# Kernel tuning notes

Measured on AMD Instinct MI355X. Metric: run time of the kernel, lower is better.

Reference implementation:

```python
import jax, jax.numpy as jnp
import numpy as np

E, K, MULT = 8, 2, 4          # num_experts, top_k, ffn mult
CF = 1.25                     # capacity_factor


def setup_inputs() -> dict:
    key = jax.random.key(0)
    ks = jax.random.split(key, 8)
    B, T, C = 4, 2048, 1024
    H = C * MULT
    s = 0.02
    return {
        "x": jax.random.normal(ks[0], (B, T, C), jnp.float32),
        "rw": jax.random.normal(ks[1], (E, C), jnp.float32) * s,   # router weight [E,C]
        "rb": jnp.zeros((E,), jnp.float32),                        # router bias
        "w1": jax.random.normal(ks[2], (E, C, H), jnp.float32) * s,
        "b1": jnp.zeros((E, H), jnp.float32),
        "w2": jax.random.normal(ks[3], (E, H, C), jnp.float32) * s,
        "b2": jnp.zeros((E, C), jnp.float32),
    }


def reference(x, rw, rb, w1, b1, w2, b2):
    B, T, C = x.shape
    N = B * T
    cap = int(CF * N / E)                      # static capacity per expert
    xf = x.reshape(N, C)
    logits = xf @ rw.T + rb                    # [N,E]
    probs = jax.nn.softmax(logits, axis=-1)
    topk_probs, topk_idx = jax.lax.top_k(probs, K)      # [N,K]
    topk_probs = topk_probs / topk_probs.sum(-1, keepdims=True)

    # Flatten (token, choice) row-major == torch.where(mask) ordering
    flat_idx = topk_idx.reshape(-1)            # [N*K] expert id per slot
    flat_gate = topk_probs.reshape(-1)         # [N*K]
    onehot = jax.nn.one_hot(flat_idx, E, dtype=jnp.int32)          # [N*K,E]
    pos = (jnp.cumsum(onehot, axis=0) - 1)[jnp.arange(N * K), flat_idx]  # rank within expert
    keep = pos < cap                           # first-come-first-served capacity drop
    tok = jnp.arange(N * K) // K               # owning token of each slot

    # Dispatch into [E, cap] buffers; dropped slots go to a dump slot at the end
    buf = jnp.where(keep, flat_idx * cap + pos, E * cap)
    gate_buf = jnp.zeros(E * cap + 1, x.dtype).at[buf].add(flat_gate)[:E * cap]
    tok_buf = jnp.zeros(E * cap + 1, jnp.int32).at[buf].set(tok)[:E * cap]

    inp = xf[tok_buf].reshape(E, cap, C)       # gathered expert inputs
    h = jax.nn.gelu(jnp.einsum('eic,ech->eih', inp, w1) + b1[:, None, :], approximate=False)
    out = jnp.einsum('eih,ehc->eic', h, w2) + b2[:, None, :]
    out = out * gate_buf.reshape(E, cap, 1)    # empty slots have gate 0 -> zero contribution

    y = jnp.zeros((N, C), x.dtype).at[tok_buf].add(out.reshape(E * cap, C))

    # Aux load-balancing loss
    imp = probs.sum(0)
    imp = imp / imp.sum()
    load = jnp.minimum(onehot.sum(0).astype(x.dtype), cap)   # kept token counts
    load = load / load.sum()
    aux_loss = (imp * load).sum() * (E ** 2)
    return y.reshape(B, T, C), aux_loss
```

## Files before the change

### kernel.cpp

```cpp
#include <hip/hip_runtime.h>
#include <hip/hip_bf16.h>
#include <math.h>

#define NE    8
#define KTOP  2
#define CDIM  1024
#define HDIM  4096
#define NTOK  8192
#define CAPE  1280
#define NSLOT (NTOK * KTOP)

typedef __bf16 bf16x8 __attribute__((ext_vector_type(8)));
typedef __bf16 bf16x4 __attribute__((ext_vector_type(4)));
typedef float  f32x4  __attribute__((ext_vector_type(4)));

#define GAS __attribute__((address_space(1)))
#define LAS __attribute__((address_space(3)))

__device__ __forceinline__ void transpose64_body(
    const float* __restrict__ src, __bf16* __restrict__ dst, int R, int Cc,
    int bx, int by, int e, int t, char* sm)
{
    __bf16 (*T)[72] = (__bf16(*)[72])sm;
    const int cb = bx * 64;
    const int rb = by * 64;
    const int px = t & 15, py = t >> 4;

    const float* s = src + (size_t)e * R * Cc
                   + (size_t)(rb + py * 4) * Cc + cb + px * 4;
    float4 m[4];
#pragma unroll
    for (int i = 0; i < 4; ++i)
        m[i] = *(const float4*)(s + (size_t)i * Cc);
#pragma unroll
    for (int j = 0; j < 4; ++j) {
        bf16x4 v;
        v[0] = (__bf16)((&m[0].x)[j]);
        v[1] = (__bf16)((&m[1].x)[j]);
        v[2] = (__bf16)((&m[2].x)[j]);
        v[3] = (__bf16)((&m[3].x)[j]);
        *(bf16x4*)&T[px * 4 + j][py * 4] = v;
    }
    __syncthreads();
    const int oc = t >> 2, rc = (t & 3) * 16;
    __bf16* d = dst + (size_t)e * R * Cc + (size_t)(cb + oc) * R + rb + rc;
    *(bf16x8*)d       = *(const bf16x8*)&T[oc][rc];
    *(bf16x8*)(d + 8) = *(const bf16x8*)&T[oc][rc + 8];
}

__global__ __launch_bounds__(256) void k_prolog(
    const float* __restrict__ w1, const float* __restrict__ w2,
    const float* __restrict__ x, const float* __restrict__ rw,
    const float* __restrict__ rb,
    __bf16* __restrict__ w1t, __bf16* __restrict__ w2t,
    float* __restrict__ probs, float* __restrict__ gates,
    int* __restrict__ tidx)
{
    __shared__ char sm[32768];
    const int bid = blockIdx.x;
    const int t   = threadIdx.x;

    if (bid < 8192) {
        const int bx = bid & 63, by = (bid >> 6) & 15, e = bid >> 10;
        transpose64_body(w1, w1t, CDIM, HDIM, bx, by, e, t, sm);
        return;
    }
    if (bid < 16384) {
        const int b2 = bid - 8192;
        const int bx = b2 & 15, by = (b2 >> 4) & 63, e = b2 >> 10;
        transpose64_body(w2, w2t, HDIM, CDIM, bx, by, e, t, sm);
        return;
    }

    float* rws = (float*)sm;
    for (int i = t; i < NE * CDIM / 4; i += 256)
        ((float4*)rws)[i] = ((const float4*)rw)[i];
    __syncthreads();

    const int wave = t >> 6, lane = t & 63;
    const int n = (bid - 16384) * 4 + wave;
    const float* xr = x + (size_t)n * CDIM;

    float acc[NE];
#pragma unroll
    for (int e = 0; e < NE; ++e) acc[e] = 0.f;
    for (int j = 0; j < CDIM / 64; ++j) {
        const float xv = xr[j * 64 + lane];
#pragma unroll
        for (int e = 0; e < NE; ++e) acc[e] += xv * rws[e * CDIM + j * 64 + lane];
    }
#pragma unroll
    for (int off = 32; off > 0; off >>= 1) {
#pragma unroll
        for (int e = 0; e < NE; ++e) acc[e] += __shfl_down(acc[e], off);
    }
    if (lane == 0) {
        float mx = -1e30f;
#pragma unroll
        for (int e = 0; e < NE; ++e) { acc[e] += rb[e]; mx = fmaxf(mx, acc[e]); }
        float p[NE], s = 0.f;
#pragma unroll
        for (int e = 0; e < NE; ++e) { p[e] = expf(acc[e] - mx); s += p[e]; }
        const float inv = 1.f / s;
#pragma unroll
        for (int e = 0; e < NE; ++e) { p[e] *= inv; probs[(size_t)n * NE + e] = p[e]; }
        int   i1 = 0;  float v1 = p[0];
        int   i2 = -1; float v2 = -1.f;
#pragma unroll
        for (int e = 1; e < NE; ++e) {
            if (p[e] > v1)      { v2 = v1; i2 = i1; v1 = p[e]; i1 = e; }
            else if (p[e] > v2) { v2 = p[e]; i2 = e; }
        }
        const float gs = 1.f / (v1 + v2);
        gates[n * 2 + 0] = v1 * gs;  gates[n * 2 + 1] = v2 * gs;
        tidx[n * 2 + 0]  = i1;       tidx[n * 2 + 1]  = i2;
    }
}

__global__ __launch_bounds__(256) void k_scan(
    const int* __restrict__ tidx, const float* __restrict__ probs,
    int* __restrict__ slot, int* __restrict__ tok, float* __restrict__ d_aux)
{
    __shared__ int   lcnt[256][NE];
    __shared__ float ps[256][NE];
    const int t = threadIdx.x;

    for (int i = t; i < NE * CAPE; i += 256) tok[i] = 0;

    int c8[NE];
#pragma unroll
    for (int e = 0; e < NE; ++e) c8[e] = 0;
    const int per  = NSLOT / 256;
    const int base = t * per;
    for (int s = 0; s < per; ++s) c8[tidx[base + s]]++;
#pragma unroll
    for (int e = 0; e < NE; ++e) lcnt[t][e] = c8[e];

    float f8[NE];
#pragma unroll
    for (int e = 0; e < NE; ++e) f8[e] = 0.f;
    for (int n = t; n < NTOK; n += 256) {
        const float4 a = *(const float4*)(probs + (size_t)n * NE);
        const float4 b = *(const float4*)(probs + (size_t)n * NE + 4);
        f8[0] += a.x; f8[1] += a.y; f8[2] += a.z; f8[3] += a.w;
        f8[4] += b.x; f8[5] += b.y; f8[6] += b.z; f8[7] += b.w;
    }
#pragma unroll
    for (int e = 0; e < NE; ++e) ps[t][e] = f8[e];

    __syncthreads();

    int run[NE];
#pragma unroll
    for (int e = 0; e < NE; ++e) run[e] = c8[e];
    for (int d = 1; d < 256; d <<= 1) {
        int add[NE];
#pragma unroll
        for (int e = 0; e < NE; ++e) add[e] = (t >= d) ? lcnt[t - d][e] : 0;
        __syncthreads();
#pragma unroll
        for (int e = 0; e < NE; ++e) { run[e] += add[e]; lcnt[t][e] = run[e]; }
        __syncthreads();
    }
    int pre[NE], tot[NE];
#pragma unroll
    for (int e = 0; e < NE; ++e) {
        pre[e] = run[e] - c8[e];
        tot[e] = lcnt[255][e];
    }

    for (int d = 128; d >= 1; d >>= 1) {
        if (t < d) {
#pragma unroll
            for (int e = 0; e < NE; ++e) ps[t][e] += ps[t + d][e];
        }
        __syncthreads();
    }

    for (int s = 0; s < per; ++s) {
        const int sg = base + s;
        const int e  = tidx[sg];
        const int p  = pre[e]++;
        if (p < CAPE) { slot[sg] = e * CAPE + p; tok[e * CAPE + p] = sg >> 1; }
        else          { slot[sg] = -1; }
    }
    if (t == 0) {
        float isum = 0.f, lsum = 0.f, ld[NE];
#pragma unroll
        for (int e = 0; e < NE; ++e) isum += ps[0][e];
#pragma unroll
        for (int e = 0; e < NE; ++e) { ld[e] = fminf((float)tot[e], (float)CAPE); lsum += ld[e]; }
        float aux = 0.f;
#pragma unroll
        for (int e = 0; e < NE; ++e) aux += (ps[0][e] / isum) * (ld[e] / lsum);
        *d_aux = aux * (float)(NE * NE);
    }
}

__global__ __launch_bounds__(256) void k_gather(
    const float* __restrict__ x, const int* __restrict__ tok,
    __bf16* __restrict__ inp)
{
    const int row = blockIdx.x;
    const int t   = threadIdx.x;
    const int tk  = tok[row];
    const float4 v = ((const float4*)(x + (size_t)tk * CDIM))[t];
    bf16x4 o;
    o[0] = (__bf16)v.x; o[1] = (__bf16)v.y; o[2] = (__bf16)v.z; o[3] = (__bf16)v.w;
    *(bf16x4*)(inp + (size_t)row * CDIM + t * 4) = o;
}

#define MFMA_BF16 __builtin_amdgcn_mfma_f32_16x16x32_bf16
#define DSR_I(dst, addr, IMM) \
    asm volatile("ds_read_b128 %0, %1 offset:" #IMM : "=v"(dst) : "v"(addr))
#define DSR(dst, addr, IMM) DSR_I(dst, addr, IMM)
#define WVM4() asm volatile("s_waitcnt vmcnt(4)" ::: "memory")
#define SB0()  __builtin_amdgcn_sched_barrier(0)

#define PH(RDB, OA0, OA1, MB, VA0, VA1, VB0, VB1, STG, VMW)                   \
    {                                                                         \
        if (RDB) {                                                            \
            DSR(fb[0][0], VB0, 0);    DSR(fb[0][1], VB1, 0);                  \
            DSR(fb[1][0], VB0, 2048); DSR(fb[1][1], VB1, 2048);               \
            DSR(fb[2][0], VB0, 4096); DSR(fb[2][1], VB1, 4096);               \
            DSR(fb[3][0], VB0, 6144); DSR(fb[3][1], VB1, 6144);               \
        }                                                                     \
        DSR(fa[0][0], VA0, OA0); DSR(fa[0][1], VA1, OA0);                     \
        DSR(fa[1][0], VA0, OA1); DSR(fa[1][1], VA1, OA1);                     \
        STG;                                                                  \
        if (RDB) { asm volatile("s_waitcnt lgkmcnt(8)" ::: "memory"); }       \
        __builtin_amdgcn_s_barrier();                                         \
        asm volatile("s_waitcnt lgkmcnt(0)" ::: "memory");                    \
        SB0();                                                                \
        __builtin_amdgcn_s_setprio(1);                                        \
        _Pragma("unroll")                                                     \
        for (int n = 0; n < 4; ++n) {                                         \
            acc[MB][n]   = MFMA_BF16(fb[n][0], fa[0][0], acc[MB][n], 0,0,0);  \
            acc[MB][n]   = MFMA_BF16(fb[n][1], fa[0][1], acc[MB][n], 0,0,0);  \
            acc[MB+1][n] = MFMA_BF16(fb[n][0], fa[1][0], acc[MB+1][n],0,0,0); \
            acc[MB+1][n] = MFMA_BF16(fb[n][1], fa[1][1], acc[MB+1][n],0,0,0); \
        }                                                                     \
        __builtin_amdgcn_s_setprio(0);                                        \
        VMW;                                                                  \
        __builtin_amdgcn_s_barrier();                                        \
        SB0();                                                                \
    }

template <bool GELU>
__global__ __launch_bounds__(512, 2) void k_gemm8(
    const __bf16* __restrict__ Aall, const __bf16* __restrict__ Ball,
    const float* __restrict__ biasAll, __bf16* __restrict__ Call,
    int Ktot, int Ntot, int NBN, int mtPerE)
{
    __shared__ char lds[133120];

    const int NK  = Ktot >> 6;
    const int NI  = NK >> 1;
    const int cpx = gridDim.x >> 3;
    const int id  = blockIdx.x;
    const int sid = (id & 7) * cpx + (id >> 3);
    const int bm  = sid / NBN, bn = sid % NBN;
    const int e   = bm / mtPerE;

    const size_t row0 = (size_t)bm * 256;
    const int    col0 = bn * 256;

    const int tid = threadIdx.x;
    const int w   = tid >> 6, l = tid & 63;
    const int wr  = w >> 2, wc = w & 3;
    const int lr  = l & 15, hi = l >> 4;

    const int srow = tid >> 3;
    const int kf   = ((tid & 7) ^ (srow & 7)) << 3;
    const __bf16* pA = Aall + (row0 + srow) * (size_t)Ktot + kf;
    const __bf16* pB = Ball + ((size_t)e * Ntot + col0 + srow) * (size_t)Ktot + kf;
    const unsigned L0 = (unsigned)(size_t)(LAS char*)lds;

    const unsigned sA00 = L0 +          w * 1024;
    const unsigned sA01 = sA00 + 16384;
    const unsigned sA10 = sA00 + 32768;
    const unsigned sA11 = sA00 + 49152;
    const unsigned sB00 = sA00 + 65536;
    const unsigned sB01 = sB00 + 16384;
    const unsigned sB10 = sB00 + 32768;
    const unsigned sB11 = sB00 + 49152;

    auto SH_A = [&](unsigned dbase, int half, int kt) {
        const __bf16* g = pA + (size_t)(half * 128) * Ktot + (size_t)kt * 64;
#pragma unroll
        for (int gg = 0; gg < 2; ++gg)
            __builtin_amdgcn_global_load_lds(
                (const GAS void*)(g + (size_t)gg * 64 * Ktot),
                (LAS void*)(size_t)(dbase + gg * 8192), 16, 0, 0);
    };
    auto SH_B = [&](unsigned dbase, int half, int kt) {
        const __bf16* g = pB + (size_t)(half * 128) * Ktot + (size_t)kt * 64;
#pragma unroll
        for (int gg = 0; gg < 2; ++gg)
            __builtin_amdgcn_global_load_lds(
                (const GAS void*)(g + (size_t)gg * 64 * Ktot),
                (LAS void*)(size_t)(dbase + gg * 8192), 16, 0, 0);
    };

    const unsigned swz = (l & 7) << 4;
    const unsigned kb0 = ((unsigned)(hi << 4)) ^ swz;
    const unsigned kb1 = ((unsigned)(64 + (hi << 4))) ^ swz;
    const unsigned vA00 = L0 + (unsigned)(wr * 16384 + lr * 128) + kb0;
    const unsigned vA01 = L0 + (unsigned)(wr * 16384 + lr * 128) + kb1;
    const unsigned vA10 = vA00 + 32768, vA11 = vA01 + 32768;
    const unsigned vBb  = L0 + 65536
        + (unsigned)((wc >> 1) * 16384 + ((wc & 1) * 64 + lr) * 128);
    const unsigned vB00 = vBb + kb0, vB01 = vBb + kb1;
    const unsigned vB10 = vB00 + 32768, vB11 = vB01 + 32768;

    SH_B(sB00, 0, 0); SH_B(sB01, 1, 0);
    SH_A(sA00, 0, 0); SH_A(sA01, 1, 0);
    SH_B(sB10, 0, 1); SH_B(sB11, 1, 1);
    WVM4();
    __builtin_amdgcn_s_barrier();
    SB0();

    f32x4 acc[8][4] = {};
    bf16x8 fa[2][2], fb[4][2];

    for (int i = 0; i < NI; ++i) {
        const int t1 = 2 * i + 1;
        const int t2 = (2 * i + 2 < NK) ? 2 * i + 2 : NK - 1;
        const int t3 = (2 * i + 3 < NK) ? 2 * i + 3 : NK - 1;
        PH(1, 0,     2048,  0, vA00, vA01, vB00, vB01, SH_A(sA10, 0, t1), (void)0)
        PH(0, 4096,  6144,  2, vA00, vA01, vB00, vB01, SH_A(sA11, 1, t1), (void)0)
        PH(0, 8192,  10240, 4, vA00, vA01, vB00, vB01, SH_B(sB00, 0, t2), (void)0)
        PH(0, 12288, 14336, 6, vA00, vA01, vB00, vB01, SH_B(sB01, 1, t2), WVM4())
        PH(1, 0,     2048,  0, vA10, vA11, vB10, vB11, SH_A(sA00, 0, t2), (void)0)
        PH(0, 4096,  6144,  2, vA10, vA11, vB10, vB11, SH_A(sA01, 1, t2), (void)0)
        PH(0, 8192,  10240, 4, vA10, vA11, vB10, vB11, SH_B(sB10, 0, t3), (void)0)
        PH(0, 12288, 14336, 6, vA10, vA11, vB10, vB11, SH_B(sB11, 1, t3), WVM4())
    }

    asm volatile("s_waitcnt vmcnt(0)" ::: "memory");
    __builtin_amdgcn_s_barrier();
    SB0();

    const int lrow0 = wr * 128;
    const int lcol0 = wc * 64;
#pragma unroll
    for (int n = 0; n < 4; ++n) {
        float bbv[4] = {0.f, 0.f, 0.f, 0.f};
        if (GELU) {
            const float4 b4 = *(const float4*)(biasAll + (size_t)e * Ntot
                                               + col0 + lcol0 + n * 16 + hi * 4);
            bbv[0] = b4.x; bbv[1] = b4.y; bbv[2] = b4.z; bbv[3] = b4.w;
        }
#pragma unroll
        for (int m = 0; m < 8; ++m) {
            const f32x4 v = acc[m][n];
            bf16x4 o;
#pragma unroll
            for (int i = 0; i < 4; ++i) {
                float t = v[i];
                if (GELU) {
                    t += bbv[i];
                    const float u  = 0.7978845608028654f * (t + 0.044715f * t * t * t);
                    const float ex = __expf(2.f * u);
                    t = t * (1.f - 1.f / (ex + 1.f));
                }
                o[i] = (__bf16)t;
            }
            *(bf16x4*)(lds + (lrow0 + m * 16 + lr) * 520
                           + (lcol0 + n * 16 + hi * 4) * 2) = o;
        }
    }
    __builtin_amdgcn_s_barrier();

    {
        const int rr0 = tid >> 5;
        const int cc  = (tid & 31) * 8;
#pragma unroll
        for (int it = 0; it < 16; ++it) {
            const int rr = it * 16 + rr0;
            const bf16x8 v = *(const bf16x8*)(lds + rr * 520 + cc * 2);
            *(bf16x8*)(Call + (row0 + rr) * (size_t)Ntot + col0 + cc) = v;
        }
    }
}

__global__ __launch_bounds__(256) void k_combine(
    const __bf16* __restrict__ outb, const int* __restrict__ slot,
    const float* __restrict__ gates, const int* __restrict__ tidx,
    const float* __restrict__ b2, float* __restrict__ y)
{
    const int n = blockIdx.x;
    const int t = threadIdx.x;
    const int c = t * 4;
    float r0 = 0.f, r1 = 0.f, r2 = 0.f, r3 = 0.f;
#pragma unroll
    for (int k = 0; k < KTOP; ++k) {
        const int s = slot[n * 2 + k];
        if (s < 0) continue;
        const float g = gates[n * 2 + k];
        const int   e = tidx[n * 2 + k];
        const bf16x4 v = *(const bf16x4*)(outb + (size_t)s * CDIM + c);
        const float4 bb = *(const float4*)(b2 + (size_t)e * CDIM + c);
        r0 += g * ((float)v[0] + bb.x);
        r1 += g * ((float)v[1] + bb.y);
        r2 += g * ((float)v[2] + bb.z);
        r3 += g * ((float)v[3] + bb.w);
    }
    float4 o = make_float4(r0, r1, r2, r3);
    *(float4*)(y + (size_t)n * CDIM + c) = o;
}

extern "C" void kernel_launch(void* const* d_in, const int* in_sizes, int n_in,
                              void* d_out, int out_size, void* d_ws, size_t ws_size,
                              hipStream_t stream)
{
    const float* x  = (const float*)d_in[0];
    const float* rw = (const float*)d_in[1];
    const float* rb = (const float*)d_in[2];
    const float* w1 = (const float*)d_in[3];
    const float* b1 = (const float*)d_in[4];
    const float* w2 = (const float*)d_in[5];
    const float* b2 = (const float*)d_in[6];
    float* y = (float*)d_out;

    char* ws = (char*)d_ws;
    size_t off = 0;
    auto alloc = [&](size_t bytes) -> void* {
        void* p = ws + off;
        off = (off + bytes + 255) & ~(size_t)255;
        return p;
    };
    __bf16* w1t  = (__bf16*)alloc((size_t)NE * CDIM * HDIM * 2);
    __bf16* w2t  = (__bf16*)alloc((size_t)NE * CDIM * HDIM * 2);
    __bf16* inp  = (__bf16*)alloc((size_t)NE * CAPE * CDIM * 2);
    __bf16* hbuf = (__bf16*)alloc((size_t)NE * CAPE * HDIM * 2);
    __bf16* outb = (__bf16*)alloc((size_t)NE * CAPE * CDIM * 2);
    float*  probs = (float*)alloc((size_t)NTOK * NE * 4);
    float*  gates = (float*)alloc((size_t)NTOK * 2 * 4);
    int*    tidx  = (int*)alloc((size_t)NTOK * 2 * 4);
    int*    slot  = (int*)alloc((size_t)NTOK * 2 * 4);
    int*    tok   = (int*)alloc((size_t)NE * CAPE * 4);

    k_prolog<<<8192 + 8192 + NTOK / 4, 256, 0, stream>>>(
        w1, w2, x, rw, rb, w1t, w2t, probs, gates, tidx);

    k_scan<<<1, 256, 0, stream>>>(tidx, probs, slot, tok, y + (size_t)NTOK * CDIM);

    k_gather<<<NE * CAPE, 256, 0, stream>>>(x, tok, inp);

    k_gemm8<true><<<dim3((NE * CAPE / 256) * (HDIM / 256)), 512, 0, stream>>>(
        inp, w1t, b1, hbuf, CDIM, HDIM, HDIM / 256, CAPE / 256);
    k_gemm8<false><<<dim3((NE * CAPE / 256) * (CDIM / 256)), 512, 0, stream>>>(
        hbuf, w2t, nullptr, outb, HDIM, CDIM, CDIM / 256, CAPE / 256);

    k_combine<<<NTOK, 256, 0, stream>>>(outb, slot, gates, tidx, b2, y);
}
```

Baseline: 373.5 us.

## Overlap w2 transpose with first expert GEMM in a combined launch

Moves the w2 fp32-to-bf16 transpose out of the prolog kernel and into the same launch as the first GEMM. Extra blocks after the 640 GEMM blocks each do two 64x64 transpose tiles. The memory-bound transpose can then fill idle CUs during the tail of the compute-bound GEMM instead of running serially before it. The cost is that transpose blocks reserve 512 threads and 133KB of LDS for a small task, which may limit their concurrency, and the GEMM body is now a macro.

```diff
diff --git a/kernel.cpp b/kernel.cpp
--- a/kernel.cpp
+++ b/kernel.cpp
@@ -9,6 +9,7 @@
 #define NTOK  8192
 #define CAPE  1280
 #define NSLOT (NTOK * KTOP)
+#define G1BLK 640
 
 typedef __bf16 bf16x8 __attribute__((ext_vector_type(8)));
 typedef __bf16 bf16x4 __attribute__((ext_vector_type(4)));
@@ -49,12 +50,10 @@
 }
 
 __global__ __launch_bounds__(256) void k_prolog(
-    const float* __restrict__ w1, const float* __restrict__ w2,
-    const float* __restrict__ x, const float* __restrict__ rw,
-    const float* __restrict__ rb,
-    __bf16* __restrict__ w1t, __bf16* __restrict__ w2t,
-    float* __restrict__ probs, float* __restrict__ gates,
-    int* __restrict__ tidx)
+    const float* __restrict__ w1, const float* __restrict__ x,
+    const float* __restrict__ rw, const float* __restrict__ rb,
+    __bf16* __restrict__ w1t, float* __restrict__ probs,
+    float* __restrict__ gates, int* __restrict__ tidx)
 {
     __shared__ char sm[32768];
     const int bid = blockIdx.x;
@@ -65,12 +64,6 @@
         transpose64_body(w1, w1t, CDIM, HDIM, bx, by, e, t, sm);
         return;
     }
-    if (bid < 16384) {
-        const int b2 = bid - 8192;
-        const int bx = b2 & 15, by = (b2 >> 4) & 63, e = b2 >> 10;
-        transpose64_body(w2, w2t, HDIM, CDIM, bx, by, e, t, sm);
-        return;
-    }
 
     float* rws = (float*)sm;
     for (int i = t; i < NE * CDIM / 4; i += 256)
@@ -78,7 +71,7 @@
     __syncthreads();
 
     const int wave = t >> 6, lane = t & 63;
-    const int n = (bid - 16384) * 4 + wave;
+    const int n = (bid - 8192) * 4 + wave;
     const float* xr = x + (size_t)n * CDIM;
 
     float acc[NE];
@@ -246,142 +239,154 @@
         SB0();                                                                \
     }
 
-template <bool GELU>
+#define GEMM_BODY(GELU_F)                                                     \
+    const int NK  = Ktot >> 6;                                                \
+    const int NI  = NK >> 1;                                                  \
+    const int bm  = sid / NBN, bn = sid % NBN;                                \
+    const int e   = bm / mtPerE;                                              \
+    const size_t row0 = (size_t)bm * 256;                                     \
+    const int    col0 = bn * 256;                                             \
+    const int tid = threadIdx.x;                                              \
+    const int w   = tid >> 6, l = tid & 63;                                   \
+    const int wr  = w >> 2, wc = w & 3;                                       \
+    const int lr  = l & 15, hi = l >> 4;                                      \
+    const int srow = tid >> 3;                                                \
+    const int kf   = ((tid & 7) ^ (srow & 7)) << 3;                           \
+    const __bf16* pA = Aall + (row0 + srow) * (size_t)Ktot + kf;              \
+    const __bf16* pB = Ball + ((size_t)e * Ntot + col0 + srow) * (size_t)Ktot + kf; \
+    const unsigned L0 = (unsigned)(size_t)(LAS char*)lds;                     \
+    const unsigned sA00 = L0 +          w * 1024;                             \
+    const unsigned sA01 = sA00 + 16384;                                       \
+    const unsigned sA10 = sA00 + 32768;                                       \
+    const unsigned sA11 = sA00 + 49152;                                       \
+    const unsigned sB00 = sA00 + 65536;                                       \
+    const unsigned sB01 = sB00 + 16384;                                       \
+    const unsigned sB10 = sB00 + 32768;                                       \
+    const unsigned sB11 = sB00 + 49152;                                       \
+    auto SH_A = [&](unsigned dbase, int half, int kt) {                       \
+        const __bf16* g = pA + (size_t)(half * 128) * Ktot + (size_t)kt * 64; \
+        _Pragma("unroll")                                                     \
+        for (int gg = 0; gg < 2; ++gg)                                        \
+            __builtin_amdgcn_global_load_lds(                                 \
+                (const GAS void*)(g + (size_t)gg * 64 * Ktot),                \
+                (LAS void*)(size_t)(dbase + gg * 8192), 16, 0, 0);            \
+    };                                                                        \
+    auto SH_B = [&](unsigned dbase, int half, int kt) {                       \
+        const __bf16* g = pB + (size_t)(half * 128) * Ktot + (size_t)kt * 64; \
+        _Pragma("unroll")                                                     \
+        for (int gg = 0; gg < 2; ++gg)                                        \
+            __builtin_amdgcn_global_load_lds(                                 \
+                (const GAS void*)(g + (size_t)gg * 64 * Ktot),                \
+                (LAS void*)(size_t)(dbase + gg * 8192), 16, 0, 0);            \
+    };                                                                        \
+    const unsigned swz = (l & 7) << 4;                                        \
+    const unsigned kb0 = ((unsigned)(hi << 4)) ^ swz;                         \
+    const unsigned kb1 = ((unsigned)(64 + (hi << 4))) ^ swz;                  \
+    const unsigned vA00 = L0 + (unsigned)(wr * 16384 + lr * 128) + kb0;       \
+    const unsigned vA01 = L0 + (unsigned)(wr * 16384 + lr * 128) + kb1;       \
+    const unsigned vA10 = vA00 + 32768, vA11 = vA01 + 32768;                  \
+    const unsigned vBb  = L0 + 65536                                          \
+        + (unsigned)((wc >> 1) * 16384 + ((wc & 1) * 64 + lr) * 128);         \
+    const unsigned vB00 = vBb + kb0, vB01 = vBb + kb1;                        \
+    const unsigned vB10 = vB00 + 32768, vB11 = vB01 + 32768;                  \
+    SH_B(sB00, 0, 0); SH_B(sB01, 1, 0);                                       \
+    SH_A(sA00, 0, 0); SH_A(sA01, 1, 0);                                       \
+    SH_B(sB10, 0, 1); SH_B(sB11, 1, 1);                                       \
+    WVM4();                                                                   \
+    __builtin_amdgcn_s_barrier();                                             \
+    SB0();                                                                    \
+    f32x4 acc[8][4] = {};                                                     \
+    bf16x8 fa[2][2], fb[4][2];                                                \
+    for (int i = 0; i < NI; ++i) {                                            \
+        const int t1 = 2 * i + 1;                                             \
+        const int t2 = (2 * i + 2 < NK) ? 2 * i + 2 : NK - 1;                 \
+        const int t3 = (2 * i + 3 < NK) ? 2 * i + 3 : NK - 1;                 \
+        PH(1, 0,     2048,  0, vA00, vA01, vB00, vB01, SH_A(sA10, 0, t1), (void)0) \
+        PH(0, 4096,  6144,  2, vA00, vA01, vB00, vB01, SH_A(sA11, 1, t1), (void)0) \
+        PH(0, 8192,  10240, 4, vA00, vA01, vB00, vB01, SH_B(sB00, 0, t2), (void)0) \
+        PH(0, 12288, 14336, 6, vA00, vA01, vB00, vB01, SH_B(sB01, 1, t2), WVM4())  \
+        PH(1, 0,     2048,  0, vA10, vA11, vB10, vB11, SH_A(sA00, 0, t2), (void)0) \
+        PH(0, 4096,  6144,  2, vA10, vA11, vB10, vB11, SH_A(sA01, 1, t2), (void)0) \
+        PH(0, 8192,  10240, 4, vA10, vA11, vB10, vB11, SH_B(sB10, 0, t3), (void)0) \
+        PH(0, 12288, 14336, 6, vA10, vA11, vB10, vB11, SH_B(sB11, 1, t3), WVM4())  \
+    }                                                                         \
+    asm volatile("s_waitcnt vmcnt(0)" ::: "memory");                          \
+    __builtin_amdgcn_s_barrier();                                             \
+    SB0();                                                                    \
+    const int lrow0 = wr * 128;                                               \
+    const int lcol0 = wc * 64;                                                \
+    _Pragma("unroll")                                                         \
+    for (int n = 0; n < 4; ++n) {                                             \
+        float bbv[4] = {0.f, 0.f, 0.f, 0.f};                                  \
+        if (GELU_F) {                                                         \
+            const float4 b4 = *(const float4*)(biasAll + (size_t)e * Ntot     \
+                                               + col0 + lcol0 + n * 16 + hi * 4); \
+            bbv[0] = b4.x; bbv[1] = b4.y; bbv[2] = b4.z; bbv[3] = b4.w;       \
+        }                                                                     \
+        _Pragma("unroll")                                                     \
+        for (int m = 0; m < 8; ++m) {                                         \
+            const f32x4 v = acc[m][n];                                        \
+            bf16x4 o;                                                         \
+            _Pragma("unroll")                                                 \
+            for (int i = 0; i < 4; ++i) {                                     \
+                float t = v[i];                                               \
+                if (GELU_F) {                                                 \
+                    t += bbv[i];                                              \
+                    const float u  = 0.7978845608028654f * (t + 0.044715f * t * t * t); \
+                    const float ex = __expf(2.f * u);                         \
+                    t = t * (1.f - 1.f / (ex + 1.f));                         \
+                }                                                             \
+                o[i] = (__bf16)t;                                             \
+            }                                                                 \
+            *(bf16x4*)(lds + (lrow0 + m * 16 + lr) * 520                      \
+                           + (lcol0 + n * 16 + hi * 4) * 2) = o;              \
+        }                                                                     \
+    }                                                                         \
+    __builtin_amdgcn_s_barrier();                                             \
+    {                                                                         \
+        const int rr0 = tid >> 5;                                             \
+        const int cc  = (tid & 31) * 8;                                       \
+        _Pragma("unroll")                                                     \
+        for (int it = 0; it < 16; ++it) {                                     \
+            const int rr = it * 16 + rr0;                                     \
+            const bf16x8 v = *(const bf16x8*)(lds + rr * 520 + cc * 2);       \
+            *(bf16x8*)(Call + (row0 + rr) * (size_t)Ntot + col0 + cc) = v;    \
+        }                                                                     \
+    }
+
+__global__ __launch_bounds__(512, 2) void k_g1w2t(
+    const __bf16* __restrict__ Aall, const __bf16* __restrict__ Ball,
+    const float* __restrict__ biasAll, __bf16* __restrict__ Call,
+    const float* __restrict__ w2, __bf16* __restrict__ w2t)
+{
+    __shared__ char lds[133120];
+
+    if (blockIdx.x < G1BLK) {
+        const int Ktot = CDIM, Ntot = HDIM, NBN = HDIM / 256, mtPerE = CAPE / 256;
+        const int id  = blockIdx.x;
+        const int sid = (id & 7) * (G1BLK >> 3) + (id >> 3);
+        GEMM_BODY(true)
+        return;
+    }
+
+    const int b2   = blockIdx.x - G1BLK;
+    const int sub  = threadIdx.x >> 8;
+    const int t    = threadIdx.x & 255;
+    const int tile = b2 * 2 + sub;
+    const int bx = tile & 15, by = (tile >> 4) & 63, e = tile >> 10;
+    transpose64_body(w2, w2t, HDIM, CDIM, bx, by, e, t, lds + sub * 9216);
+}
+
 __global__ __launch_bounds__(512, 2) void k_gemm8(
     const __bf16* __restrict__ Aall, const __bf16* __restrict__ Ball,
     const float* __restrict__ biasAll, __bf16* __restrict__ Call,
     int Ktot, int Ntot, int NBN, int mtPerE)
 {
     __shared__ char lds[133120];
-
-    const int NK  = Ktot >> 6;
-    const int NI  = NK >> 1;
     const int cpx = gridDim.x >> 3;
     const int id  = blockIdx.x;
     const int sid = (id & 7) * cpx + (id >> 3);
-    const int bm  = sid / NBN, bn = sid % NBN;
-    const int e   = bm / mtPerE;
-
-    const size_t row0 = (size_t)bm * 256;
-    const int    col0 = bn * 256;
-
-    const int tid = threadIdx.x;
-    const int w   = tid >> 6, l = tid & 63;
-    const int wr  = w >> 2, wc = w & 3;
-    const int lr  = l & 15, hi = l >> 4;
-
-    const int srow = tid >> 3;
-    const int kf   = ((tid & 7) ^ (srow & 7)) << 3;
-    const __bf16* pA = Aall + (row0 + srow) * (size_t)Ktot + kf;
-    const __bf16* pB = Ball + ((size_t)e * Ntot + col0 + srow) * (size_t)Ktot + kf;
-    const unsigned L0 = (unsigned)(size_t)(LAS char*)lds;
-
-    const unsigned sA00 = L0 +          w * 1024;
-    const unsigned sA01 = sA00 + 16384;
-    const unsigned sA10 = sA00 + 32768;
-    const unsigned sA11 = sA00 + 49152;
-    const unsigned sB00 = sA00 + 65536;
-    const unsigned sB01 = sB00 + 16384;
-    const unsigned sB10 = sB00 + 32768;
-    const unsigned sB11 = sB00 + 49152;
-
-    auto SH_A = [&](unsigned dbase, int half, int kt) {
-        const __bf16* g = pA + (size_t)(half * 128) * Ktot + (size_t)kt * 64;
-#pragma unroll
-        for (int gg = 0; gg < 2; ++gg)
-            __builtin_amdgcn_global_load_lds(
-                (const GAS void*)(g + (size_t)gg * 64 * Ktot),
-                (LAS void*)(size_t)(dbase + gg * 8192), 16, 0, 0);
-    };
-    auto SH_B = [&](unsigned dbase, int half, int kt) {
-        const __bf16* g = pB + (size_t)(half * 128) * Ktot + (size_t)kt * 64;
-#pragma unroll
-        for (int gg = 0; gg < 2; ++gg)
-            __builtin_amdgcn_global_load_lds(
-                (const GAS void*)(g + (size_t)gg * 64 * Ktot),
-                (LAS void*)(size_t)(dbase + gg * 8192), 16, 0, 0);
-    };
-
-    const unsigned swz = (l & 7) << 4;
-    const unsigned kb0 = ((unsigned)(hi << 4)) ^ swz;
-    const unsigned kb1 = ((unsigned)(64 + (hi << 4))) ^ swz;
-    const unsigned vA00 = L0 + (unsigned)(wr * 16384 + lr * 128) + kb0;
-    const unsigned vA01 = L0 + (unsigned)(wr * 16384 + lr * 128) + kb1;
-    const unsigned vA10 = vA00 + 32768, vA11 = vA01 + 32768;
-    const unsigned vBb  = L0 + 65536
-        + (unsigned)((wc >> 1) * 16384 + ((wc & 1) * 64 + lr) * 128);
-    const unsigned vB00 = vBb + kb0, vB01 = vBb + kb1;
-    const unsigned vB10 = vB00 + 32768, vB11 = vB01 + 32768;
-
-    SH_B(sB00, 0, 0); SH_B(sB01, 1, 0);
-    SH_A(sA00, 0, 0); SH_A(sA01, 1, 0);
-    SH_B(sB10, 0, 1); SH_B(sB11, 1, 1);
-    WVM4();
-    __builtin_amdgcn_s_barrier();
-    SB0();
-
-    f32x4 acc[8][4] = {};
-    bf16x8 fa[2][2], fb[4][2];
-
-    for (int i = 0; i < NI; ++i) {
-        const int t1 = 2 * i + 1;
-        const int t2 = (2 * i + 2 < NK) ? 2 * i + 2 : NK - 1;
-        const int t3 = (2 * i + 3 < NK) ? 2 * i + 3 : NK - 1;
-        PH(1, 0,     2048,  0, vA00, vA01, vB00, vB01, SH_A(sA10, 0, t1), (void)0)
-        PH(0, 4096,  6144,  2, vA00, vA01, vB00, vB01, SH_A(sA11, 1, t1), (void)0)
-        PH(0, 8192,  10240, 4, vA00, vA01, vB00, vB01, SH_B(sB00, 0, t2), (void)0)
-        PH(0, 12288, 14336, 6, vA00, vA01, vB00, vB01, SH_B(sB01, 1, t2), WVM4())
-        PH(1, 0,     2048,  0, vA10, vA11, vB10, vB11, SH_A(sA00, 0, t2), (void)0)
-        PH(0, 4096,  6144,  2, vA10, vA11, vB10, vB11, SH_A(sA01, 1, t2), (void)0)
-        PH(0, 8192,  10240, 4, vA10, vA11, vB10, vB11, SH_B(sB10, 0, t3), (void)0)
-        PH(0, 12288, 14336, 6, vA10, vA11, vB10, vB11, SH_B(sB11, 1, t3), WVM4())
-    }
-
-    asm volatile("s_waitcnt vmcnt(0)" ::: "memory");
-    __builtin_amdgcn_s_barrier();
-    SB0();
-
-    const int lrow0 = wr * 128;
-    const int lcol0 = wc * 64;
-#pragma unroll
-    for (int n = 0; n < 4; ++n) {
-        float bbv[4] = {0.f, 0.f, 0.f, 0.f};
-        if (GELU) {
-            const float4 b4 = *(const float4*)(biasAll + (size_t)e * Ntot
-                                               + col0 + lcol0 + n * 16 + hi * 4);
-            bbv[0] = b4.x; bbv[1] = b4.y; bbv[2] = b4.z; bbv[3] = b4.w;
-        }
-#pragma unroll
-        for (int m = 0; m < 8; ++m) {
-            const f32x4 v = acc[m][n];
-            bf16x4 o;
-#pragma unroll
-            for (int i = 0; i < 4; ++i) {
-                float t = v[i];
-                if (GELU) {
-                    t += bbv[i];
-                    const float u  = 0.7978845608028654f * (t + 0.044715f * t * t * t);
-                    const float ex = __expf(2.f * u);
-                    t = t * (1.f - 1.f / (ex + 1.f));
-                }
-                o[i] = (__bf16)t;
-            }
-            *(bf16x4*)(lds + (lrow0 + m * 16 + lr) * 520
-                           + (lcol0 + n * 16 + hi * 4) * 2) = o;
-        }
-    }
-    __builtin_amdgcn_s_barrier();
-
-    {
-        const int rr0 = tid >> 5;
-        const int cc  = (tid & 31) * 8;
-#pragma unroll
-        for (int it = 0; it < 16; ++it) {
-            const int rr = it * 16 + rr0;
-            const bf16x8 v = *(const bf16x8*)(lds + rr * 520 + cc * 2);
-            *(bf16x8*)(Call + (row0 + rr) * (size_t)Ntot + col0 + cc) = v;
-        }
-    }
+    GEMM_BODY(false)
 }
 
 __global__ __launch_bounds__(256) void k_combine(
@@ -441,16 +446,16 @@
     int*    slot  = (int*)alloc((size_t)NTOK * 2 * 4);
     int*    tok   = (int*)alloc((size_t)NE * CAPE * 4);
 
-    k_prolog<<<8192 + 8192 + NTOK / 4, 256, 0, stream>>>(
-        w1, w2, x, rw, rb, w1t, w2t, probs, gates, tidx);
+    k_prolog<<<8192 + NTOK / 4, 256, 0, stream>>>(
+        w1, x, rw, rb, w1t, probs, gates, tidx);
 
     k_scan<<<1, 256, 0, stream>>>(tidx, probs, slot, tok, y + (size_t)NTOK * CDIM);
 
     k_gather<<<NE * CAPE, 256, 0, stream>>>(x, tok, inp);
 
-    k_gemm8<true><<<dim3((NE * CAPE / 256) * (HDIM / 256)), 512, 0, stream>>>(
-        inp, w1t, b1, hbuf, CDIM, HDIM, HDIM / 256, CAPE / 256);
-    k_gemm8<false><<<dim3((NE * CAPE / 256) * (CDIM / 256)), 512, 0, stream>>>(
+    k_g1w2t<<<G1BLK + 4096, 512, 0, stream>>>(inp, w1t, b1, hbuf, w2, w2t);
+
+    k_gemm8<<<dim3((NE * CAPE / 256) * (CDIM / 256)), 512, 0, stream>>>(
         hbuf, w2t, nullptr, outb, HDIM, CDIM, CDIM / 256, CAPE / 256);
 
     k_combine<<<NTOK, 256, 0, stream>>>(outb, slot, gates, tidx, b2, y);
```

After: 354.7 us. 5.0% less time.
